# Performance work log

Measured on AMD Instinct MI355X. Metric: run time of the kernel, lower is better.

## Reference

```python
import jax, jax.numpy as jnp
import numpy as np

X_DIM, Y_DIM, SEQ_LEN, BATCH = 50, 6, 230, 16384

def _dw_conv1d(x, w, b):
    # x: [B, C, L], w: [C, k], b: [C]; depthwise (groups=C) valid conv
    out = jax.lax.conv_general_dilated(
        x, w[:, None, :],  # rhs [C_out=C, C_in/groups=1, k]
        window_strides=(1,), padding='VALID',
        feature_group_count=x.shape[1],
        dimension_numbers=('NCW', 'OIW', 'NCW'))
    return out + b[None, :, None]

def setup_inputs() -> dict:
    key = jax.random.key(0)
    ks = jax.random.split(key, 9)
    f = lambda k, s, scale: (jax.random.normal(k, s, dtype=jnp.float32) * scale)
    return {
        'sequence': f(ks[0], (BATCH, SEQ_LEN, X_DIM), 1.0),
        'w1': f(ks[1], (X_DIM, 3), 1.0 / np.sqrt(3)),
        'b1': f(ks[2], (X_DIM,), 0.1),
        'w2': f(ks[3], (X_DIM, 6), 1.0 / np.sqrt(6)),
        'b2': f(ks[4], (X_DIM,), 0.1),
        'w3': f(ks[5], (X_DIM, 12), 1.0 / np.sqrt(12)),
        'b3': f(ks[6], (X_DIM,), 0.1),
        'w_out': f(ks[7], (Y_DIM * SEQ_LEN, 3 * X_DIM), 1.0 / np.sqrt(3 * X_DIM)),
        'b_out': f(ks[8], (Y_DIM * SEQ_LEN,), 0.1),
    }

def reference(sequence, w1, b1, w2, b2, w3, b3, w_out, b_out):
    # sequence: [B, 230, x_dim] -> [B, x_dim, 230]
    seq = jnp.transpose(sequence, (0, 2, 1))
    # Each conv+maxpool pair reduces to max over the full conv output length.
    m1 = jnp.max(_dw_conv1d(seq, w1, b1), axis=-1)  # [B, x_dim]
    m2 = jnp.max(_dw_conv1d(seq, w2, b2), axis=-1)
    m3 = jnp.max(_dw_conv1d(seq, w3, b3), axis=-1)
    # torch cat order is per-feature interleaved: (c1_f, c2_f, c3_f) for each f
    flat = jnp.stack([m1, m2, m3], axis=-1).reshape(seq.shape[0], 3 * X_DIM)
    out = flat @ w_out.T + b_out  # [B, y_dim*230]
    return out.reshape(-1, SEQ_LEN, Y_DIM)
```

## Files before the change

### kernel.cpp

```cpp
#include <hip/hip_runtime.h>
#include <math.h>

#define X_DIM   50
#define SEQ_LEN 230
#define BATCH   16384
#define KTRUE   150
#define KPAD    160
#define NOUT    1380
#define NPAD    1408

__global__ __launch_bounds__(256) void prep_w(const float* __restrict__ w,
                                              float* __restrict__ wp) {
    int i = blockIdx.x * 256 + threadIdx.x;
    int n = i / KPAD;
    int k = i - n * KPAD;
    float v = 0.f;
    if (n < NOUT && k < KTRUE) v = w[n * KTRUE + k];
    wp[i] = v;
}

__global__ __launch_bounds__(256) void conv_max(
    const float* __restrict__ x,
    const float* __restrict__ w1, const float* __restrict__ b1,
    const float* __restrict__ w2, const float* __restrict__ b2,
    const float* __restrict__ w3, const float* __restrict__ b3,
    float* __restrict__ flat) {
    int g = blockIdx.x * 256 + threadIdx.x;
    int b = g / X_DIM;
    int c = g - b * X_DIM;

    const float* p = x + (size_t)b * (SEQ_LEN * X_DIM) + c;

    float W1c[3], W2c[6], W3c[12];
#pragma unroll
    for (int i = 0; i < 3; ++i)  W1c[i] = w1[c * 3 + i];
#pragma unroll
    for (int i = 0; i < 6; ++i)  W2c[i] = w2[c * 6 + i];
#pragma unroll
    for (int i = 0; i < 12; ++i) W3c[i] = w3[c * 12 + i];

    float m1 = -1e30f, m2 = -1e30f, m3 = -1e30f;
    float buf[12];

#pragma unroll
    for (int t = 0; t < 12; ++t) {
        float v = p[t * X_DIM];
        buf[t] = v;
        if (t >= 2) {
            float s = fmaf(buf[t - 2], W1c[0], fmaf(buf[t - 1], W1c[1], v * W1c[2]));
            m1 = fmaxf(m1, s);
        }
        if (t >= 5) {
            float s = 0.f;
#pragma unroll
            for (int i = 0; i < 6; ++i) s = fmaf(buf[t - 5 + i], W2c[i], s);
            m2 = fmaxf(m2, s);
        }
        if (t == 11) {
            float s = 0.f;
#pragma unroll
            for (int i = 0; i < 12; ++i) s = fmaf(buf[i], W3c[i], s);
            m3 = fmaxf(m3, s);
        }
    }

    const float* q = p + 12 * X_DIM;
#pragma unroll 2
    for (int it = 0; it < 18; ++it) {
#pragma unroll
        for (int j = 0; j < 12; ++j) {
            float v = q[j * X_DIM];
            buf[j] = v;
            float s1 = fmaf(buf[(j + 10) % 12], W1c[0],
                       fmaf(buf[(j + 11) % 12], W1c[1], v * W1c[2]));
            m1 = fmaxf(m1, s1);
            float s2 = 0.f;
#pragma unroll
            for (int i = 0; i < 6; ++i) s2 = fmaf(buf[(j + 7 + i) % 12], W2c[i], s2);
            m2 = fmaxf(m2, s2);
            float s3 = 0.f;
#pragma unroll
            for (int i = 0; i < 12; ++i) s3 = fmaf(buf[(j + 1 + i) % 12], W3c[i], s3);
            m3 = fmaxf(m3, s3);
        }
        q += 12 * X_DIM;
    }

#pragma unroll
    for (int j = 0; j < 2; ++j) {
        float v = q[j * X_DIM];
        buf[j] = v;
        float s1 = fmaf(buf[(j + 10) % 12], W1c[0],
                   fmaf(buf[(j + 11) % 12], W1c[1], v * W1c[2]));
        m1 = fmaxf(m1, s1);
        float s2 = 0.f;
#pragma unroll
        for (int i = 0; i < 6; ++i) s2 = fmaf(buf[(j + 7 + i) % 12], W2c[i], s2);
        m2 = fmaxf(m2, s2);
        float s3 = 0.f;
#pragma unroll
        for (int i = 0; i < 12; ++i) s3 = fmaf(buf[(j + 1 + i) % 12], W3c[i], s3);
        m3 = fmaxf(m3, s3);
    }

    size_t base = (size_t)b * KPAD + 3 * c;
    flat[base + 0] = m1 + b1[c];
    flat[base + 1] = m2 + b2[c];
    flat[base + 2] = m3 + b3[c];
    if (c < KPAD - KTRUE) flat[(size_t)b * KPAD + KTRUE + c] = 0.f;
}

#define BM 128
#define BN 128
#define BK 16

__global__ __launch_bounds__(256) void gemm_k(
    const float* __restrict__ A,
    const float* __restrict__ Wp,
    const float* __restrict__ bias,
    float* __restrict__ out) {
    __shared__ float As[BK][BM];
    __shared__ float Bs[BK][BN];

    int tid = threadIdx.x;
    int bn = blockIdx.x * BN;
    int bm = blockIdx.y * BM;
    int tm = tid >> 4;
    int tn = tid & 15;

    int lrow = tid >> 2;
    int lk4  = (tid & 3) * 4;

    const float* Ap = A  + (size_t)(bm + lrow) * KPAD + lk4;
    const float* Bp = Wp + (size_t)(bn + lrow) * KPAD + lk4;

    float acc[8][8] = {};

    for (int k0 = 0; k0 < KPAD; k0 += BK) {
        float4 a0 = *(const float4*)(Ap + k0);
        float4 a1 = *(const float4*)(Ap + (size_t)64 * KPAD + k0);
        float4 bb0 = *(const float4*)(Bp + k0);
        float4 bb1 = *(const float4*)(Bp + (size_t)64 * KPAD + k0);

        __syncthreads();
        As[lk4 + 0][lrow] = a0.x;  As[lk4 + 1][lrow] = a0.y;
        As[lk4 + 2][lrow] = a0.z;  As[lk4 + 3][lrow] = a0.w;
        As[lk4 + 0][lrow + 64] = a1.x;  As[lk4 + 1][lrow + 64] = a1.y;
        As[lk4 + 2][lrow + 64] = a1.z;  As[lk4 + 3][lrow + 64] = a1.w;
        Bs[lk4 + 0][lrow] = bb0.x;  Bs[lk4 + 1][lrow] = bb0.y;
        Bs[lk4 + 2][lrow] = bb0.z;  Bs[lk4 + 3][lrow] = bb0.w;
        Bs[lk4 + 0][lrow + 64] = bb1.x;  Bs[lk4 + 1][lrow + 64] = bb1.y;
        Bs[lk4 + 2][lrow + 64] = bb1.z;  Bs[lk4 + 3][lrow + 64] = bb1.w;
        __syncthreads();

#pragma unroll
        for (int k = 0; k < BK; ++k) {
            float4 av0 = *(const float4*)&As[k][tm * 8];
            float4 av1 = *(const float4*)&As[k][tm * 8 + 4];
            float4 bv0 = *(const float4*)&Bs[k][tn * 8];
            float4 bv1 = *(const float4*)&Bs[k][tn * 8 + 4];
            float a[8] = {av0.x, av0.y, av0.z, av0.w, av1.x, av1.y, av1.z, av1.w};
            float bfr[8] = {bv0.x, bv0.y, bv0.z, bv0.w, bv1.x, bv1.y, bv1.z, bv1.w};
#pragma unroll
            for (int i = 0; i < 8; ++i)
#pragma unroll
                for (int jj = 0; jj < 8; ++jj)
                    acc[i][jj] = fmaf(a[i], bfr[jj], acc[i][jj]);
        }
    }

#pragma unroll
    for (int i = 0; i < 8; ++i) {
        size_t m = (size_t)(bm + tm * 8 + i);
#pragma unroll
        for (int j4 = 0; j4 < 8; j4 += 4) {
            int n = bn + tn * 8 + j4;
            if (n < NOUT) {
                float4 r;
                r.x = acc[i][j4 + 0] + bias[n + 0];
                r.y = acc[i][j4 + 1] + bias[n + 1];
                r.z = acc[i][j4 + 2] + bias[n + 2];
                r.w = acc[i][j4 + 3] + bias[n + 3];
                *(float4*)(out + m * NOUT + n) = r;
            }
        }
    }
}

extern "C" void kernel_launch(void* const* d_in, const int* in_sizes, int n_in,
                              void* d_out, int out_size, void* d_ws, size_t ws_size,
                              hipStream_t stream) {
    const float* seq   = (const float*)d_in[0];
    const float* w1    = (const float*)d_in[1];
    const float* b1    = (const float*)d_in[2];
    const float* w2    = (const float*)d_in[3];
    const float* b2    = (const float*)d_in[4];
    const float* w3    = (const float*)d_in[5];
    const float* b3    = (const float*)d_in[6];
    const float* w_out = (const float*)d_in[7];
    const float* b_out = (const float*)d_in[8];
    float* out = (float*)d_out;

    float* flat = (float*)d_ws;
    float* wp   = flat + (size_t)BATCH * KPAD;

    prep_w<<<(NPAD * KPAD) / 256, 256, 0, stream>>>(w_out, wp);
    conv_max<<<(BATCH * X_DIM) / 256, 256, 0, stream>>>(
        seq, w1, b1, w2, b2, w3, b3, flat);
    gemm_k<<<dim3(NPAD / BN, BATCH / BM), 256, 0, stream>>>(flat, wp, b_out, out);
}
```

Measured before the change: 1.080 ms.

## Pack conv channels into float2 and double-buffer the GEMM shared tiles

The depthwise conv+max kernel now has each thread handle two adjacent channels. It uses 2-wide float vectors so loads are 8-byte and the FMAs can map to packed fp32 instructions, and it launches half as many threads. The GEMM switches to double-buffered LDS tiles: global loads for the next K chunk are issued before computing the current one, which leaves one barrier per chunk instead of two. It also remaps each thread's output columns to two 4-wide groups 64 apart, aiming to reduce LDS bank conflicts on B reads and to simplify the store bounds check. The costs are higher register pressure per conv thread, fewer conv threads, and double the GEMM shared memory, which may lower occupancy.

Result: slower. 1.129 ms (+4.5%).

```diff
diff --git a/kernel.cpp b/kernel.cpp
--- a/kernel.cpp
+++ b/kernel.cpp
@@ -8,6 +8,12 @@
 #define KPAD    160
 #define NOUT    1380
 #define NPAD    1408
+
+typedef float v2f __attribute__((ext_vector_type(2)));
+
+__device__ __forceinline__ v2f vmax2(v2f a, v2f b) {
+    v2f r; r.x = fmaxf(a.x, b.x); r.y = fmaxf(a.y, b.y); return r;
+}
 
 __global__ __launch_bounds__(256) void prep_w(const float* __restrict__ w,
                                               float* __restrict__ wp) {
@@ -26,101 +32,105 @@
     const float* __restrict__ w3, const float* __restrict__ b3,
     float* __restrict__ flat) {
     int g = blockIdx.x * 256 + threadIdx.x;
-    int b = g / X_DIM;
-    int c = g - b * X_DIM;
-
-    const float* p = x + (size_t)b * (SEQ_LEN * X_DIM) + c;
-
-    float W1c[3], W2c[6], W3c[12];
-#pragma unroll
-    for (int i = 0; i < 3; ++i)  W1c[i] = w1[c * 3 + i];
-#pragma unroll
-    for (int i = 0; i < 6; ++i)  W2c[i] = w2[c * 6 + i];
-#pragma unroll
-    for (int i = 0; i < 12; ++i) W3c[i] = w3[c * 12 + i];
-
-    float m1 = -1e30f, m2 = -1e30f, m3 = -1e30f;
-    float buf[12];
+    int b = g / 25;
+    int cp = g - b * 25;
+    int c0 = 2 * cp;
+    int c1 = c0 + 1;
+
+    const v2f* p = reinterpret_cast<const v2f*>(x + (size_t)b * (SEQ_LEN * X_DIM)) + cp;
+
+    v2f W1c[3], W2c[6], W3c[12];
+#pragma unroll
+    for (int i = 0; i < 3; ++i)  { W1c[i].x = w1[c0 * 3 + i];  W1c[i].y = w1[c1 * 3 + i]; }
+#pragma unroll
+    for (int i = 0; i < 6; ++i)  { W2c[i].x = w2[c0 * 6 + i];  W2c[i].y = w2[c1 * 6 + i]; }
+#pragma unroll
+    for (int i = 0; i < 12; ++i) { W3c[i].x = w3[c0 * 12 + i]; W3c[i].y = w3[c1 * 12 + i]; }
+
+    v2f m1 = {-1e30f, -1e30f}, m2 = m1, m3 = m1;
+    v2f buf[12];
 
 #pragma unroll
     for (int t = 0; t < 12; ++t) {
-        float v = p[t * X_DIM];
+        v2f v = p[t * 25];
         buf[t] = v;
         if (t >= 2) {
-            float s = fmaf(buf[t - 2], W1c[0], fmaf(buf[t - 1], W1c[1], v * W1c[2]));
-            m1 = fmaxf(m1, s);
+            v2f s = buf[t - 2] * W1c[0] + buf[t - 1] * W1c[1] + v * W1c[2];
+            m1 = vmax2(m1, s);
         }
         if (t >= 5) {
-            float s = 0.f;
-#pragma unroll
-            for (int i = 0; i < 6; ++i) s = fmaf(buf[t - 5 + i], W2c[i], s);
-            m2 = fmaxf(m2, s);
+            v2f s = buf[t - 5] * W2c[0];
+#pragma unroll
+            for (int i = 1; i < 6; ++i) s += buf[t - 5 + i] * W2c[i];
+            m2 = vmax2(m2, s);
         }
         if (t == 11) {
-            float s = 0.f;
-#pragma unroll
-            for (int i = 0; i < 12; ++i) s = fmaf(buf[i], W3c[i], s);
-            m3 = fmaxf(m3, s);
-        }
-    }
-
-    const float* q = p + 12 * X_DIM;
+            v2f s = buf[0] * W3c[0];
+#pragma unroll
+            for (int i = 1; i < 12; ++i) s += buf[i] * W3c[i];
+            m3 = vmax2(m3, s);
+        }
+    }
+
+    const v2f* q = p + 12 * 25;
 #pragma unroll 2
     for (int it = 0; it < 18; ++it) {
 #pragma unroll
         for (int j = 0; j < 12; ++j) {
-            float v = q[j * X_DIM];
+            v2f v = q[j * 25];
             buf[j] = v;
-            float s1 = fmaf(buf[(j + 10) % 12], W1c[0],
-                       fmaf(buf[(j + 11) % 12], W1c[1], v * W1c[2]));
-            m1 = fmaxf(m1, s1);
-            float s2 = 0.f;
-#pragma unroll
-            for (int i = 0; i < 6; ++i) s2 = fmaf(buf[(j + 7 + i) % 12], W2c[i], s2);
-            m2 = fmaxf(m2, s2);
-            float s3 = 0.f;
-#pragma unroll
-            for (int i = 0; i < 12; ++i) s3 = fmaf(buf[(j + 1 + i) % 12], W3c[i], s3);
-            m3 = fmaxf(m3, s3);
-        }
-        q += 12 * X_DIM;
+            v2f s1 = buf[(j + 10) % 12] * W1c[0] + buf[(j + 11) % 12] * W1c[1] + v * W1c[2];
+            m1 = vmax2(m1, s1);
+            v2f s2 = buf[(j + 7) % 12] * W2c[0];
+#pragma unroll
+            for (int i = 1; i < 6; ++i) s2 += buf[(j + 7 + i) % 12] * W2c[i];
+            m2 = vmax2(m2, s2);
+            v2f s3 = buf[(j + 1) % 12] * W3c[0];
+#pragma unroll
+            for (int i = 1; i < 12; ++i) s3 += buf[(j + 1 + i) % 12] * W3c[i];
+            m3 = vmax2(m3, s3);
+        }
+        q += 12 * 25;
     }
 
 #pragma unroll
     for (int j = 0; j < 2; ++j) {
-        float v = q[j * X_DIM];
+        v2f v = q[j * 25];
         buf[j] = v;
-        float s1 = fmaf(buf[(j + 10) % 12], W1c[0],
-                   fmaf(buf[(j + 11) % 12], W1c[1], v * W1c[2]));
-        m1 = fmaxf(m1, s1);
-        float s2 = 0.f;
-#pragma unroll
-        for (int i = 0; i < 6; ++i) s2 = fmaf(buf[(j + 7 + i) % 12], W2c[i], s2);
-        m2 = fmaxf(m2, s2);
-        float s3 = 0.f;
-#pragma unroll
-        for (int i = 0; i < 12; ++i) s3 = fmaf(buf[(j + 1 + i) % 12], W3c[i], s3);
-        m3 = fmaxf(m3, s3);
-    }
-
-    size_t base = (size_t)b * KPAD + 3 * c;
-    flat[base + 0] = m1 + b1[c];
-    flat[base + 1] = m2 + b2[c];
-    flat[base + 2] = m3 + b3[c];
-    if (c < KPAD - KTRUE) flat[(size_t)b * KPAD + KTRUE + c] = 0.f;
+        v2f s1 = buf[(j + 10) % 12] * W1c[0] + buf[(j + 11) % 12] * W1c[1] + v * W1c[2];
+        m1 = vmax2(m1, s1);
+        v2f s2 = buf[(j + 7) % 12] * W2c[0];
+#pragma unroll
+        for (int i = 1; i < 6; ++i) s2 += buf[(j + 7 + i) % 12] * W2c[i];
+        m2 = vmax2(m2, s2);
+        v2f s3 = buf[(j + 1) % 12] * W3c[0];
+#pragma unroll
+        for (int i = 1; i < 12; ++i) s3 += buf[(j + 1 + i) % 12] * W3c[i];
+        m3 = vmax2(m3, s3);
+    }
+
+    size_t base = (size_t)b * KPAD + 6 * cp;
+    flat[base + 0] = m1.x + b1[c0];
+    flat[base + 1] = m2.x + b2[c0];
+    flat[base + 2] = m3.x + b3[c0];
+    flat[base + 3] = m1.y + b1[c1];
+    flat[base + 4] = m2.y + b2[c1];
+    flat[base + 5] = m3.y + b3[c1];
+    if (cp < KPAD - KTRUE) flat[(size_t)b * KPAD + KTRUE + cp] = 0.f;
 }
 
 #define BM 128
 #define BN 128
 #define BK 16
+#define NCHUNK (KPAD / BK)
 
 __global__ __launch_bounds__(256) void gemm_k(
     const float* __restrict__ A,
     const float* __restrict__ Wp,
     const float* __restrict__ bias,
     float* __restrict__ out) {
-    __shared__ float As[BK][BM];
-    __shared__ float Bs[BK][BN];
+    __shared__ float As[2][BK][BM];
+    __shared__ float Bs[2][BK][BN];
 
     int tid = threadIdx.x;
     int bn = blockIdx.x * BN;
@@ -136,53 +146,81 @@
 
     float acc[8][8] = {};
 
-    for (int k0 = 0; k0 < KPAD; k0 += BK) {
-        float4 a0 = *(const float4*)(Ap + k0);
-        float4 a1 = *(const float4*)(Ap + (size_t)64 * KPAD + k0);
-        float4 bb0 = *(const float4*)(Bp + k0);
-        float4 bb1 = *(const float4*)(Bp + (size_t)64 * KPAD + k0);
-
+    {
+        float4 a0  = *(const float4*)(Ap);
+        float4 a1  = *(const float4*)(Ap + (size_t)64 * KPAD);
+        float4 c0  = *(const float4*)(Bp);
+        float4 c1  = *(const float4*)(Bp + (size_t)64 * KPAD);
+        As[0][lk4 + 0][lrow] = a0.x;  As[0][lk4 + 1][lrow] = a0.y;
+        As[0][lk4 + 2][lrow] = a0.z;  As[0][lk4 + 3][lrow] = a0.w;
+        As[0][lk4 + 0][lrow + 64] = a1.x;  As[0][lk4 + 1][lrow + 64] = a1.y;
+        As[0][lk4 + 2][lrow + 64] = a1.z;  As[0][lk4 + 3][lrow + 64] = a1.w;
+        Bs[0][lk4 + 0][lrow] = c0.x;  Bs[0][lk4 + 1][lrow] = c0.y;
+        Bs[0][lk4 + 2][lrow] = c0.z;  Bs[0][lk4 + 3][lrow] = c0.w;
+        Bs[0][lk4 + 0][lrow + 64] = c1.x;  Bs[0][lk4 + 1][lrow + 64] = c1.y;
+        Bs[0][lk4 + 2][lrow + 64] = c1.z;  Bs[0][lk4 + 3][lrow + 64] = c1.w;
         __syncthreads();
-        As[lk4 + 0][lrow] = a0.x;  As[lk4 + 1][lrow] = a0.y;
-        As[lk4 + 2][lrow] = a0.z;  As[lk4 + 3][lrow] = a0.w;
-        As[lk4 + 0][lrow + 64] = a1.x;  As[lk4 + 1][lrow + 64] = a1.y;
-        As[lk4 + 2][lrow + 64] = a1.z;  As[lk4 + 3][lrow + 64] = a1.w;
-        Bs[lk4 + 0][lrow] = bb0.x;  Bs[lk4 + 1][lrow] = bb0.y;
-        Bs[lk4 + 2][lrow] = bb0.z;  Bs[lk4 + 3][lrow] = bb0.w;
-        Bs[lk4 + 0][lrow + 64] = bb1.x;  Bs[lk4 + 1][lrow + 64] = bb1.y;
-        Bs[lk4 + 2][lrow + 64] = bb1.z;  Bs[lk4 + 3][lrow + 64] = bb1.w;
-        __syncthreads();
+    }
+
+    for (int k0 = 0; k0 < NCHUNK; ++k0) {
+        int cur = k0 & 1;
+
+        float4 a0, a1, c0, c1;
+        if (k0 < NCHUNK - 1) {
+            int off = (k0 + 1) * BK;
+            a0 = *(const float4*)(Ap + off);
+            a1 = *(const float4*)(Ap + (size_t)64 * KPAD + off);
+            c0 = *(const float4*)(Bp + off);
+            c1 = *(const float4*)(Bp + (size_t)64 * KPAD + off);
+        }
 
 #pragma unroll
         for (int k = 0; k < BK; ++k) {
-            float4 av0 = *(const float4*)&As[k][tm * 8];
-            float4 av1 = *(const float4*)&As[k][tm * 8 + 4];
-            float4 bv0 = *(const float4*)&Bs[k][tn * 8];
-            float4 bv1 = *(const float4*)&Bs[k][tn * 8 + 4];
-            float a[8] = {av0.x, av0.y, av0.z, av0.w, av1.x, av1.y, av1.z, av1.w};
-            float bfr[8] = {bv0.x, bv0.y, bv0.z, bv0.w, bv1.x, bv1.y, bv1.z, bv1.w};
+            float4 av0 = *(const float4*)&As[cur][k][tm * 8];
+            float4 av1 = *(const float4*)&As[cur][k][tm * 8 + 4];
+            float4 bv0 = *(const float4*)&Bs[cur][k][tn * 4];
+            float4 bv1 = *(const float4*)&Bs[cur][k][tn * 4 + 64];
+            float a[8]  = {av0.x, av0.y, av0.z, av0.w, av1.x, av1.y, av1.z, av1.w};
+            float bf[8] = {bv0.x, bv0.y, bv0.z, bv0.w, bv1.x, bv1.y, bv1.z, bv1.w};
 #pragma unroll
             for (int i = 0; i < 8; ++i)
 #pragma unroll
                 for (int jj = 0; jj < 8; ++jj)
-                    acc[i][jj] = fmaf(a[i], bfr[jj], acc[i][jj]);
+                    acc[i][jj] = fmaf(a[i], bf[jj], acc[i][jj]);
+        }
+
+        if (k0 < NCHUNK - 1) {
+            int nxt = cur ^ 1;
+            As[nxt][lk4 + 0][lrow] = a0.x;  As[nxt][lk4 + 1][lrow] = a0.y;
+            As[nxt][lk4 + 2][lrow] = a0.z;  As[nxt][lk4 + 3][lrow] = a0.w;
+            As[nxt][lk4 + 0][lrow + 64] = a1.x;  As[nxt][lk4 + 1][lrow + 64] = a1.y;
+            As[nxt][lk4 + 2][lrow + 64] = a1.z;  As[nxt][lk4 + 3][lrow + 64] = a1.w;
+            Bs[nxt][lk4 + 0][lrow] = c0.x;  Bs[nxt][lk4 + 1][lrow] = c0.y;
+            Bs[nxt][lk4 + 2][lrow] = c0.z;  Bs[nxt][lk4 + 3][lrow] = c0.w;
+            Bs[nxt][lk4 + 0][lrow + 64] = c1.x;  Bs[nxt][lk4 + 1][lrow + 64] = c1.y;
+            Bs[nxt][lk4 + 2][lrow + 64] = c1.z;  Bs[nxt][lk4 + 3][lrow + 64] = c1.w;
+            __syncthreads();
         }
     }
 
 #pragma unroll
     for (int i = 0; i < 8; ++i) {
         size_t m = (size_t)(bm + tm * 8 + i);
-#pragma unroll
-        for (int j4 = 0; j4 < 8; j4 += 4) {
-            int n = bn + tn * 8 + j4;
-            if (n < NOUT) {
-                float4 r;
-                r.x = acc[i][j4 + 0] + bias[n + 0];
-                r.y = acc[i][j4 + 1] + bias[n + 1];
-                r.z = acc[i][j4 + 2] + bias[n + 2];
-                r.w = acc[i][j4 + 3] + bias[n + 3];
-                *(float4*)(out + m * NOUT + n) = r;
-            }
+        int n0 = bn + tn * 4;
+        float4 r0;
+        r0.x = acc[i][0] + bias[n0 + 0];
+        r0.y = acc[i][1] + bias[n0 + 1];
+        r0.z = acc[i][2] + bias[n0 + 2];
+        r0.w = acc[i][3] + bias[n0 + 3];
+        *(float4*)(out + m * NOUT + n0) = r0;
+        int n1 = bn + 64 + tn * 4;
+        if (n1 < NOUT) {
+            float4 r1;
+            r1.x = acc[i][4] + bias[n1 + 0];
+            r1.y = acc[i][5] + bias[n1 + 1];
+            r1.z = acc[i][6] + bias[n1 + 2];
+            r1.w = acc[i][7] + bias[n1 + 3];
+            *(float4*)(out + m * NOUT + n1) = r1;
         }
     }
 }
@@ -205,7 +243,7 @@
     float* wp   = flat + (size_t)BATCH * KPAD;
 
     prep_w<<<(NPAD * KPAD) / 256, 256, 0, stream>>>(w_out, wp);
-    conv_max<<<(BATCH * X_DIM) / 256, 256, 0, stream>>>(
+    conv_max<<<(BATCH * 25) / 256, 256, 0, stream>>>(
         seq, w1, b1, w2, b2, w3, b3, flat);
     gemm_k<<<dim3(NPAD / BN, BATCH / BM), 256, 0, stream>>>(flat, wp, b_out, out);
 }
```
